# Optimization experiments

Measured on AMD Instinct MI355X. Metric: run time of the kernel, lower is better.

The kernel has to match this reference:

```python
import jax, jax.numpy as jnp
import numpy as np
import math

IN_FEATURES = 3072
PADDED = 4096  # next power of two
ACT_BITS = 8
LN_EPS = 1e-6


def hadamard_transform(x):
    """Normalized fast Walsh-Hadamard transform along last dim (power of 2)."""
    n = x.shape[-1]
    m = n.bit_length() - 1  # log2(n)
    shape = x.shape
    y = x.reshape(shape[:-1] + (2,) * m)
    for ax in range(len(shape) - 1, len(shape) - 1 + m):
        a = jnp.take(y, 0, axis=ax)
        b = jnp.take(y, 1, axis=ax)
        y = jnp.stack([a + b, a - b], axis=ax)
    return y.reshape(shape) / jnp.sqrt(jnp.asarray(n, x.dtype))


def activation_quant(x, bits=ACT_BITS):
    """Per-token absmax int-b quant with STE (BitNet style)."""
    qb = 2 ** (bits - 1) - 1  # 127
    scale = qb / jnp.clip(jnp.max(jnp.abs(x), axis=-1, keepdims=True), 1e-5)
    q = jnp.clip(jnp.round(x * scale), -qb - 1, qb) / scale
    return x + jax.lax.stop_gradient(q - x)


def weight_quant(w):
    """Ternary absmean weight quant with STE (as in training path)."""
    scale = jnp.clip(jnp.mean(jnp.abs(w)), 1e-5)
    q = jnp.clip(jnp.round(w / scale), -1.0, 1.0) * scale
    return w + jax.lax.stop_gradient(q - w)


def layer_norm(x, gamma, beta, eps=LN_EPS):
    mu = jnp.mean(x, axis=-1, keepdims=True)
    var = jnp.mean(jnp.square(x - mu), axis=-1, keepdims=True)
    return (x - mu) * jax.lax.rsqrt(var + eps) * gamma + beta


def setup_inputs() -> dict:
    key = jax.random.key(0)
    k1, k2 = jax.random.split(key)
    x = jax.random.normal(k1, (4, 2048, IN_FEATURES), dtype=jnp.float32)
    ln_gamma = jnp.ones((IN_FEATURES,), dtype=jnp.float32)
    ln_beta = jnp.zeros((IN_FEATURES,), dtype=jnp.float32)
    weight = jax.random.normal(k2, (4096, PADDED), dtype=jnp.float32) * 0.02
    return {"x": x, "ln_gamma": ln_gamma, "ln_beta": ln_beta, "weight": weight}


def reference(x, ln_gamma, ln_beta, weight):
    x_norm = layer_norm(x, ln_gamma, ln_beta)
    pad = PADDED - IN_FEATURES
    x_pad = jnp.pad(x_norm, ((0, 0), (0, 0), (0, pad)))
    x_had = hadamard_transform(x_pad)
    x_q = activation_quant(x_had)
    w_q = weight_quant(weight)
    # F.linear: x @ W^T
    out = jnp.einsum('bsd,od->bso', x_q, w_q)
    return out
```

## Files before the change

kernel.cpp:

```cpp
#include <hip/hip_runtime.h>
#include <stdint.h>

#define TOKENS 8192
#define IN_F   3072
#define PAD_F  4096
#define N_OUT  4096
#define K_DIM  4096

using i32x4 = __attribute__((ext_vector_type(4))) int;

#define Q_OFF    0
#define WQ_OFF   33554432
#define AINV_OFF 50331648
#define PART_OFF 50364416
#define WSC_OFF  50380800

__device__ __forceinline__ void gload_lds16(const void* g, void* l) {
    __builtin_amdgcn_global_load_lds(
        (__attribute__((address_space(1))) void*)(void*)g,
        (__attribute__((address_space(3))) void*)l,
        16, 0, 0);
}

__global__ __launch_bounds__(256) void k_wabs(const float* __restrict__ w,
                                              float* __restrict__ partial) {
    int tid = threadIdx.x;
    const float4* w4 = (const float4*)(w + (size_t)blockIdx.x * 4096);
    float s = 0.f;
#pragma unroll
    for (int i = 0; i < 4; ++i) {
        float4 v = w4[tid + i * 256];
        s += fabsf(v.x) + fabsf(v.y) + fabsf(v.z) + fabsf(v.w);
    }
#pragma unroll
    for (int o = 32; o > 0; o >>= 1) s += __shfl_xor(s, o);
    __shared__ float rb[4];
    if ((tid & 63) == 0) rb[tid >> 6] = s;
    __syncthreads();
    if (tid == 0) partial[blockIdx.x] = rb[0] + rb[1] + rb[2] + rb[3];
}

__global__ __launch_bounds__(256) void k_wscale(const float* __restrict__ partial,
                                                float* __restrict__ wsp) {
    int tid = threadIdx.x;
    float s = 0.f;
#pragma unroll
    for (int i = 0; i < 16; ++i) s += partial[tid + i * 256];
#pragma unroll
    for (int o = 32; o > 0; o >>= 1) s += __shfl_xor(s, o);
    __shared__ float rb[4];
    if ((tid & 63) == 0) rb[tid >> 6] = s;
    __syncthreads();
    if (tid == 0)
        wsp[0] = fmaxf((rb[0] + rb[1] + rb[2] + rb[3]) * (1.0f / 16777216.0f), 1e-5f);
}

__global__ __launch_bounds__(256) void k_wquant(const float* __restrict__ w,
                                                const float* __restrict__ wsp,
                                                unsigned int* __restrict__ wq) {
    int idx = blockIdx.x * 256 + threadIdx.x;
    float ws = wsp[0];
    float4 v = ((const float4*)w)[idx];
    int a = (int)rintf(v.x / ws); a = max(-1, min(1, a));
    int b = (int)rintf(v.y / ws); b = max(-1, min(1, b));
    int c = (int)rintf(v.z / ws); c = max(-1, min(1, c));
    int d = (int)rintf(v.w / ws); d = max(-1, min(1, d));
    unsigned int p = (unsigned)(a & 255) | ((unsigned)(b & 255) << 8) |
                     ((unsigned)(c & 255) << 16) | ((unsigned)(d & 255) << 24);
    wq[idx] = p;
}

__global__ __launch_bounds__(256) void k_lnfwht(const float* __restrict__ x,
                                                const float* __restrict__ gamma,
                                                const float* __restrict__ beta,
                                                signed char* __restrict__ q,
                                                float* __restrict__ ainv) {
    __shared__ float s[PAD_F];
    __shared__ float rb[8];
    int tid = threadIdx.x;
    int lane = tid & 63;
    int t = blockIdx.x;
    const float* xr = x + (size_t)t * IN_F;

    float v[16];
    float sum = 0.f;
#pragma unroll
    for (int i = 0; i < 12; ++i) { v[i] = xr[tid + i * 256]; sum += v[i]; }
    v[12] = v[13] = v[14] = v[15] = 0.f;
#pragma unroll
    for (int o = 32; o > 0; o >>= 1) sum += __shfl_xor(sum, o);
    if ((tid & 63) == 0) rb[tid >> 6] = sum;
    __syncthreads();
    float mu = (rb[0] + rb[1] + rb[2] + rb[3]) * (1.0f / 3072.0f);

    float s2 = 0.f;
#pragma unroll
    for (int i = 0; i < 12; ++i) { float d = v[i] - mu; s2 += d * d; }
#pragma unroll
    for (int o = 32; o > 0; o >>= 1) s2 += __shfl_xor(s2, o);
    if ((tid & 63) == 0) rb[4 + (tid >> 6)] = s2;
    __syncthreads();
    float var = (rb[4] + rb[5] + rb[6] + rb[7]) * (1.0f / 3072.0f);
    float rstd = 1.0f / sqrtf(var + 1e-6f);

#pragma unroll
    for (int i = 0; i < 12; ++i)
        v[i] = (v[i] - mu) * rstd * gamma[tid + i * 256] + beta[tid + i * 256];

#pragma unroll
    for (int b = 1; b < 16; b <<= 1) {
#pragma unroll
        for (int i = 0; i < 16; ++i) {
            if (!(i & b)) {
                float a0 = v[i], b0 = v[i | b];
                v[i] = a0 + b0;
                v[i | b] = a0 - b0;
            }
        }
    }
#pragma unroll
    for (int m = 1; m <= 32; m <<= 1) {
#pragma unroll
        for (int i = 0; i < 16; ++i) {
            float p = __shfl_xor(v[i], m);
            v[i] = (lane & m) ? (p - v[i]) : (v[i] + p);
        }
    }
#pragma unroll
    for (int m = 64; m <= 128; m <<= 1) {
        __syncthreads();
#pragma unroll
        for (int i = 0; i < 16; ++i) s[tid + i * 256] = v[i];
        __syncthreads();
#pragma unroll
        for (int i = 0; i < 16; ++i) {
            float p = s[(tid ^ m) + i * 256];
            v[i] = (tid & m) ? (p - v[i]) : (v[i] + p);
        }
    }

    float mx = 0.f;
#pragma unroll
    for (int i = 0; i < 16; ++i) mx = fmaxf(mx, fabsf(v[i]));
#pragma unroll
    for (int o = 32; o > 0; o >>= 1) mx = fmaxf(mx, __shfl_xor(mx, o));
    __syncthreads();
    if ((tid & 63) == 0) rb[tid >> 6] = mx;
    __syncthreads();
    float amraw = fmaxf(fmaxf(rb[0], rb[1]), fmaxf(rb[2], rb[3]));
    float amax = fmaxf(amraw * (1.0f / 64.0f), 1e-5f);
    float scale = 127.0f / amax;
    if (tid == 0) ainv[t] = amax * (1.0f / 127.0f);

    signed char* qr = q + (size_t)t * PAD_F;
#pragma unroll
    for (int i = 0; i < 16; ++i) {
        int qi = (int)rintf(v[i] * (1.0f / 64.0f) * scale);
        qi = max(-128, min(127, qi));
        qr[tid + i * 256] = (signed char)qi;
    }
}

#define BK 64
#define NT (K_DIM / BK)

#define VMW(n) asm volatile("s_waitcnt vmcnt(" #n ")" ::: "memory")

__global__ __launch_bounds__(512, 2) void k_gemm(const signed char* __restrict__ Aq,
                                                 const signed char* __restrict__ Wq,
                                                 const float* __restrict__ ainv,
                                                 const float* __restrict__ wsp,
                                                 float* __restrict__ out) {
    __shared__ signed char sA[4][128 * 128];
    __shared__ signed char sB[4][128 * 128];

    int tid = threadIdx.x;
    int lane = tid & 63, wid = tid >> 6;

    int bid = blockIdx.x;
    int xcd = bid & 7, li = bid >> 3;
    int bmb = xcd * 4 + (li & 3);
    int bnb = li >> 2;
    size_t bm0 = (size_t)bmb * 256, bn0 = (size_t)bnb * 256;

    int wm = wid >> 2, wn = wid & 3;

    int rr = lane >> 3, pp = lane & 7;
    int Lg = pp ^ rr;
    int spar = Lg >> 2, sh = Lg & 3;
    const signed char* gA = Aq + (bm0 + (size_t)(wid * 32 + 2 * rr + spar)) * K_DIM + sh * 16;
    const signed char* gB = Wq + (bn0 + (size_t)(wid * 32 + 2 * rr + spar)) * K_DIM + sh * 16;

    int fr = lane & 15, hh = lane >> 4;
    int pos = (((fr & 1) << 2) | hh) ^ (fr >> 1);
    int abase = (wm * 64 + (fr >> 1)) * 8 + pos;
    int bbase = (wn * 32 + (fr >> 1)) * 8 + pos;

    i32x4 acc[8][4];
#pragma unroll
    for (int m = 0; m < 8; ++m)
#pragma unroll
        for (int n = 0; n < 4; ++n) acc[m][n] = (i32x4){0, 0, 0, 0};

    i32x4 afA[8], bfA[4], afB[8], bfB[4];

    auto STAGE = [&](int b, int t) {
        size_t k0 = (size_t)t * BK;
        gload_lds16(gA + k0, &sA[b][(wid * 16) * 128]);
        gload_lds16(gA + k0 + (size_t)16 * K_DIM, &sA[b][(wid * 16 + 8) * 128]);
        gload_lds16(gB + k0, &sB[b][(wid * 16) * 128]);
        gload_lds16(gB + k0 + (size_t)16 * K_DIM, &sB[b][(wid * 16 + 8) * 128]);
    };

#define LOADF(B, AF, BF) do {                                           \
    const i32x4* va = (const i32x4*)&sA[B][0];                          \
    const i32x4* vb = (const i32x4*)&sB[B][0];                          \
    _Pragma("unroll")                                                   \
    for (int mf = 0; mf < 8; ++mf) AF[mf] = va[abase + mf * 64];        \
    _Pragma("unroll")                                                   \
    for (int nf = 0; nf < 4; ++nf) BF[nf] = vb[bbase + nf * 64];        \
} while (0)

#define COMPUTE(AF, BF) do {                                            \
    __builtin_amdgcn_s_setprio(1);                                      \
    _Pragma("unroll")                                                   \
    for (int mf = 0; mf < 8; ++mf)                                      \
        _Pragma("unroll")                                               \
        for (int nf = 0; nf < 4; ++nf)                                  \
            acc[mf][nf] = __builtin_amdgcn_mfma_i32_16x16x64_i8(        \
                AF[mf], BF[nf], acc[mf][nf], 0, 0, 0);                  \
    __builtin_amdgcn_s_setprio(0);                                      \
} while (0)

#define BODY(T, AFC, BFC, AFN, BFN) do {                                \
    STAGE((T + 3) & 3, T + 3);                                          \
    VMW(8);                                                             \
    __builtin_amdgcn_sched_barrier(0);                                  \
    __builtin_amdgcn_s_barrier();                                       \
    __builtin_amdgcn_sched_barrier(0);                                  \
    LOADF((T + 1) & 3, AFN, BFN);                                       \
    COMPUTE(AFC, BFC);                                                  \
    asm volatile("s_waitcnt lgkmcnt(0)" ::: "memory");                  \
    __builtin_amdgcn_sched_barrier(0);                                  \
} while (0)

    STAGE(0, 0);
    STAGE(1, 1);
    STAGE(2, 2);
    VMW(8);
    __builtin_amdgcn_sched_barrier(0);
    __builtin_amdgcn_s_barrier();
    __builtin_amdgcn_sched_barrier(0);
    LOADF(0, afA, bfA);
    asm volatile("s_waitcnt lgkmcnt(0)" ::: "memory");
    __builtin_amdgcn_sched_barrier(0);

#pragma unroll 1
    for (int t = 0; t < NT - 4; t += 2) {
        BODY(t, afA, bfA, afB, bfB);
        BODY(t + 1, afB, bfB, afA, bfA);
    }
    BODY(NT - 4, afA, bfA, afB, bfB);
    VMW(4);
    __builtin_amdgcn_sched_barrier(0);
    __builtin_amdgcn_s_barrier();
    __builtin_amdgcn_sched_barrier(0);
    LOADF(2, afA, bfA);
    COMPUTE(afB, bfB);
    asm volatile("s_waitcnt lgkmcnt(0)" ::: "memory");
    __builtin_amdgcn_sched_barrier(0);
    VMW(0);
    __builtin_amdgcn_sched_barrier(0);
    __builtin_amdgcn_s_barrier();
    __builtin_amdgcn_sched_barrier(0);
    LOADF(3, afB, bfB);
    COMPUTE(afA, bfA);
    asm volatile("s_waitcnt lgkmcnt(0)" ::: "memory");
    __builtin_amdgcn_sched_barrier(0);
    COMPUTE(afB, bfB);

    float wsc = wsp[0];
#pragma unroll
    for (int mf = 0; mf < 8; ++mf) {
        size_t row0 = bm0 + wm * 128 + mf * 16 + hh * 4;
#pragma unroll
        for (int r = 0; r < 4; ++r) {
            size_t row = row0 + r;
            float sa = wsc * ainv[row];
#pragma unroll
            for (int nf = 0; nf < 4; ++nf) {
                size_t col = bn0 + wn * 64 + nf * 16 + fr;
                out[row * N_OUT + col] = (float)acc[mf][nf][r] * sa;
            }
        }
    }
#undef LOADF
#undef COMPUTE
#undef BODY
}

extern "C" void kernel_launch(void* const* d_in, const int* in_sizes, int n_in,
                              void* d_out, int out_size, void* d_ws, size_t ws_size,
                              hipStream_t stream) {
    const float* x     = (const float*)d_in[0];
    const float* gamma = (const float*)d_in[1];
    const float* beta  = (const float*)d_in[2];
    const float* w     = (const float*)d_in[3];
    float* out = (float*)d_out;
    char* ws = (char*)d_ws;

    signed char* q   = (signed char*)(ws + Q_OFF);
    signed char* wq  = (signed char*)(ws + WQ_OFF);
    float* ainv      = (float*)(ws + AINV_OFF);
    float* partial   = (float*)(ws + PART_OFF);
    float* wsp       = (float*)(ws + WSC_OFF);

    k_wabs<<<dim3(4096), dim3(256), 0, stream>>>(w, partial);
    k_wscale<<<dim3(1), dim3(256), 0, stream>>>(partial, wsp);
    k_wquant<<<dim3(16384), dim3(256), 0, stream>>>(w, wsp, (unsigned int*)wq);
    k_lnfwht<<<dim3(TOKENS), dim3(256), 0, stream>>>(x, gamma, beta, q, ainv);
    k_gemm<<<dim3(512), dim3(512), 0, stream>>>(q, wq, ainv, wsp, out);
}
```

Measured before the change: 213.4 us.

## Use 4 waves with 128x128 warp tiles and interleave LDS loads with MFMAs

Cuts the GEMM block from 8 waves to 4, so each wave computes a 128x128 sub-tile (8x8 MFMA fragments) with larger accumulator and fragment arrays, and each wave issues twice as many global-to-LDS loads. The fragment loads for the next K-step are split into four chunks, each placed between groups of 16 MFMAs, and the pipeline tail is rewritten as conditional body steps. The goal is higher fragment reuse per wave and better overlap of LDS reads with matrix math. The cost is roughly doubled VGPR/AGPR pressure with launch bounds of one block, fewer waves per CU to hide latency, and a risk of spills.

```diff
diff --git a/kernel.cpp b/kernel.cpp
--- a/kernel.cpp
+++ b/kernel.cpp
@@ -165,8 +165,9 @@
 #define NT (K_DIM / BK)
 
 #define VMW(n) asm volatile("s_waitcnt vmcnt(" #n ")" ::: "memory")
-
-__global__ __launch_bounds__(512, 2) void k_gemm(const signed char* __restrict__ Aq,
+#define SB0()  __builtin_amdgcn_sched_barrier(0)
+
+__global__ __launch_bounds__(256, 1) void k_gemm(const signed char* __restrict__ Aq,
                                                  const signed char* __restrict__ Wq,
                                                  const float* __restrict__ ainv,
                                                  const float* __restrict__ wsp,
@@ -183,101 +184,99 @@
     int bnb = li >> 2;
     size_t bm0 = (size_t)bmb * 256, bn0 = (size_t)bnb * 256;
 
-    int wm = wid >> 2, wn = wid & 3;
+    int wm = wid >> 1, wn = wid & 1;
 
     int rr = lane >> 3, pp = lane & 7;
     int Lg = pp ^ rr;
     int spar = Lg >> 2, sh = Lg & 3;
-    const signed char* gA = Aq + (bm0 + (size_t)(wid * 32 + 2 * rr + spar)) * K_DIM + sh * 16;
-    const signed char* gB = Wq + (bn0 + (size_t)(wid * 32 + 2 * rr + spar)) * K_DIM + sh * 16;
+    const signed char* gA = Aq + (bm0 + (size_t)(wid * 64 + 2 * rr + spar)) * K_DIM + sh * 16;
+    const signed char* gB = Wq + (bn0 + (size_t)(wid * 64 + 2 * rr + spar)) * K_DIM + sh * 16;
 
     int fr = lane & 15, hh = lane >> 4;
     int pos = (((fr & 1) << 2) | hh) ^ (fr >> 1);
     int abase = (wm * 64 + (fr >> 1)) * 8 + pos;
-    int bbase = (wn * 32 + (fr >> 1)) * 8 + pos;
-
-    i32x4 acc[8][4];
+    int bbase = (wn * 64 + (fr >> 1)) * 8 + pos;
+
+    i32x4 acc[8][8];
 #pragma unroll
     for (int m = 0; m < 8; ++m)
 #pragma unroll
-        for (int n = 0; n < 4; ++n) acc[m][n] = (i32x4){0, 0, 0, 0};
-
-    i32x4 afA[8], bfA[4], afB[8], bfB[4];
+        for (int n = 0; n < 8; ++n) acc[m][n] = (i32x4){0, 0, 0, 0};
+
+    i32x4 afA[8], bfA[8], afB[8], bfB[8];
 
     auto STAGE = [&](int b, int t) {
         size_t k0 = (size_t)t * BK;
-        gload_lds16(gA + k0, &sA[b][(wid * 16) * 128]);
-        gload_lds16(gA + k0 + (size_t)16 * K_DIM, &sA[b][(wid * 16 + 8) * 128]);
-        gload_lds16(gB + k0, &sB[b][(wid * 16) * 128]);
-        gload_lds16(gB + k0 + (size_t)16 * K_DIM, &sB[b][(wid * 16 + 8) * 128]);
+#pragma unroll
+        for (int i = 0; i < 4; ++i) {
+            gload_lds16(gA + k0 + (size_t)i * 16 * K_DIM, &sA[b][(wid * 32 + i * 8) * 128]);
+            gload_lds16(gB + k0 + (size_t)i * 16 * K_DIM, &sB[b][(wid * 32 + i * 8) * 128]);
+        }
     };
 
-#define LOADF(B, AF, BF) do {                                           \
-    const i32x4* va = (const i32x4*)&sA[B][0];                          \
-    const i32x4* vb = (const i32x4*)&sB[B][0];                          \
+#define LOAD4(VP, BASE, AF, LO) do {                                    \
+    AF[LO]     = VP[BASE + (LO) * 64];                                  \
+    AF[LO + 1] = VP[BASE + (LO + 1) * 64];                              \
+    AF[LO + 2] = VP[BASE + (LO + 2) * 64];                              \
+    AF[LO + 3] = VP[BASE + (LO + 3) * 64];                              \
+} while (0)
+
+#define MFMA16(AF, BF, M0) do {                                         \
     _Pragma("unroll")                                                   \
-    for (int mf = 0; mf < 8; ++mf) AF[mf] = va[abase + mf * 64];        \
-    _Pragma("unroll")                                                   \
-    for (int nf = 0; nf < 4; ++nf) BF[nf] = vb[bbase + nf * 64];        \
+    for (int nf = 0; nf < 8; ++nf) {                                    \
+        acc[M0][nf] = __builtin_amdgcn_mfma_i32_16x16x64_i8(            \
+            AF[M0], BF[nf], acc[M0][nf], 0, 0, 0);                      \
+        acc[M0 + 1][nf] = __builtin_amdgcn_mfma_i32_16x16x64_i8(        \
+            AF[M0 + 1], BF[nf], acc[M0 + 1][nf], 0, 0, 0);              \
+    }                                                                   \
 } while (0)
 
-#define COMPUTE(AF, BF) do {                                            \
-    __builtin_amdgcn_s_setprio(1);                                      \
-    _Pragma("unroll")                                                   \
-    for (int mf = 0; mf < 8; ++mf)                                      \
-        _Pragma("unroll")                                               \
-        for (int nf = 0; nf < 4; ++nf)                                  \
-            acc[mf][nf] = __builtin_amdgcn_mfma_i32_16x16x64_i8(        \
-                AF[mf], BF[nf], acc[mf][nf], 0, 0, 0);                  \
-    __builtin_amdgcn_s_setprio(0);                                      \
-} while (0)
-
-#define BODY(T, AFC, BFC, AFN, BFN) do {                                \
-    STAGE((T + 3) & 3, T + 3);                                          \
-    VMW(8);                                                             \
-    __builtin_amdgcn_sched_barrier(0);                                  \
+#define BODYC(T, NW, DS, AFC, BFC, AFN, BFN) do {                       \
+    if (DS) STAGE((T + 3) & 3, T + 3);                                  \
+    VMW(NW);                                                            \
+    SB0();                                                              \
     __builtin_amdgcn_s_barrier();                                       \
-    __builtin_amdgcn_sched_barrier(0);                                  \
-    LOADF((T + 1) & 3, AFN, BFN);                                       \
-    COMPUTE(AFC, BFC);                                                  \
+    SB0();                                                              \
+    const i32x4* va = (const i32x4*)&sA[(T + 1) & 3][0];                \
+    const i32x4* vb = (const i32x4*)&sB[(T + 1) & 3][0];                \
+    LOAD4(va, abase, AFN, 0); SB0(); MFMA16(AFC, BFC, 0); SB0();        \
+    LOAD4(va, abase, AFN, 4); SB0(); MFMA16(AFC, BFC, 2); SB0();        \
+    LOAD4(vb, bbase, BFN, 0); SB0(); MFMA16(AFC, BFC, 4); SB0();        \
+    LOAD4(vb, bbase, BFN, 4); SB0(); MFMA16(AFC, BFC, 6); SB0();        \
     asm volatile("s_waitcnt lgkmcnt(0)" ::: "memory");                  \
-    __builtin_amdgcn_sched_barrier(0);                                  \
+    SB0();                                                              \
 } while (0)
 
     STAGE(0, 0);
     STAGE(1, 1);
     STAGE(2, 2);
-    VMW(8);
-    __builtin_amdgcn_sched_barrier(0);
+    VMW(16);
+    SB0();
     __builtin_amdgcn_s_barrier();
-    __builtin_amdgcn_sched_barrier(0);
-    LOADF(0, afA, bfA);
+    SB0();
+    {
+        const i32x4* va = (const i32x4*)&sA[0][0];
+        const i32x4* vb = (const i32x4*)&sB[0][0];
+        LOAD4(va, abase, afA, 0);
+        LOAD4(va, abase, afA, 4);
+        LOAD4(vb, bbase, bfA, 0);
+        LOAD4(vb, bbase, bfA, 4);
+    }
     asm volatile("s_waitcnt lgkmcnt(0)" ::: "memory");
-    __builtin_amdgcn_sched_barrier(0);
+    SB0();
 
 #pragma unroll 1
     for (int t = 0; t < NT - 4; t += 2) {
-        BODY(t, afA, bfA, afB, bfB);
-        BODY(t + 1, afB, bfB, afA, bfA);
-    }
-    BODY(NT - 4, afA, bfA, afB, bfB);
-    VMW(4);
-    __builtin_amdgcn_sched_barrier(0);
-    __builtin_amdgcn_s_barrier();
-    __builtin_amdgcn_sched_barrier(0);
-    LOADF(2, afA, bfA);
-    COMPUTE(afB, bfB);
-    asm volatile("s_waitcnt lgkmcnt(0)" ::: "memory");
-    __builtin_amdgcn_sched_barrier(0);
-    VMW(0);
-    __builtin_amdgcn_sched_barrier(0);
-    __builtin_amdgcn_s_barrier();
-    __builtin_amdgcn_sched_barrier(0);
-    LOADF(3, afB, bfB);
-    COMPUTE(afA, bfA);
-    asm volatile("s_waitcnt lgkmcnt(0)" ::: "memory");
-    __builtin_amdgcn_sched_barrier(0);
-    COMPUTE(afB, bfB);
+        BODYC(t, 16, true, afA, bfA, afB, bfB);
+        BODYC(t + 1, 16, true, afB, bfB, afA, bfA);
+    }
+    BODYC(NT - 4, 16, true, afA, bfA, afB, bfB);
+    BODYC(NT - 3, 8, false, afB, bfB, afA, bfA);
+    BODYC(NT - 2, 0, false, afA, bfA, afB, bfB);
+    MFMA16(afB, bfB, 0);
+    MFMA16(afB, bfB, 2);
+    MFMA16(afB, bfB, 4);
+    MFMA16(afB, bfB, 6);
 
     float wsc = wsp[0];
 #pragma unroll
@@ -288,15 +287,15 @@
             size_t row = row0 + r;
             float sa = wsc * ainv[row];
 #pragma unroll
-            for (int nf = 0; nf < 4; ++nf) {
-                size_t col = bn0 + wn * 64 + nf * 16 + fr;
+            for (int nf = 0; nf < 8; ++nf) {
+                size_t col = bn0 + wn * 128 + nf * 16 + fr;
                 out[row * N_OUT + col] = (float)acc[mf][nf][r] * sa;
             }
         }
     }
-#undef LOADF
-#undef COMPUTE
-#undef BODY
+#undef LOAD4
+#undef MFMA16
+#undef BODYC
 }
 
 extern "C" void kernel_launch(void* const* d_in, const int* in_sizes, int n_in,
@@ -319,5 +318,5 @@
     k_wscale<<<dim3(1), dim3(256), 0, stream>>>(partial, wsp);
     k_wquant<<<dim3(16384), dim3(256), 0, stream>>>(w, wsp, (unsigned int*)wq);
     k_lnfwht<<<dim3(TOKENS), dim3(256), 0, stream>>>(x, gamma, beta, q, ainv);
-    k_gemm<<<dim3(512), dim3(512), 0, stream>>>(q, wq, ainv, wsp, out);
-}
+    k_gemm<<<dim3(512), dim3(256), 0, stream>>>(q, wq, ainv, wsp, out);
+}
```

New measurement: 229.9 us. 7.7% more time.

## Shrink GEMM tile to 256x128, triple-buffer LDS, drop register double-buffering

Applied to the files above, without the earlier changes.

The int8 GEMM block tile drops from 256x256 to 256x128, with 2x4 waves each owning a 64x64 subtile, and the grid doubles to 1024 blocks. LDS staging goes from four buffers to three and the B tile is halved, and the register-level double buffering of fragments is replaced by a simple load-then-compute per K step. The aim is higher occupancy (launch bounds 512,4), less register pressure and LDS use, and more blocks to fill the CUs. The cost is lower arithmetic intensity per block, more global traffic for A, and less overlap of LDS reads with MFMA work.

```diff
diff --git a/kernel.cpp b/kernel.cpp
--- a/kernel.cpp
+++ b/kernel.cpp
@@ -165,14 +165,15 @@
 #define NT (K_DIM / BK)
 
 #define VMW(n) asm volatile("s_waitcnt vmcnt(" #n ")" ::: "memory")
-
-__global__ __launch_bounds__(512, 2) void k_gemm(const signed char* __restrict__ Aq,
+#define SB0()  __builtin_amdgcn_sched_barrier(0)
+
+__global__ __launch_bounds__(512, 4) void k_gemm(const signed char* __restrict__ Aq,
                                                  const signed char* __restrict__ Wq,
                                                  const float* __restrict__ ainv,
                                                  const float* __restrict__ wsp,
                                                  float* __restrict__ out) {
-    __shared__ signed char sA[4][128 * 128];
-    __shared__ signed char sB[4][128 * 128];
+    __shared__ signed char sA[3][128 * 128];
+    __shared__ signed char sB[3][64 * 128];
 
     int tid = threadIdx.x;
     int lane = tid & 63, wid = tid >> 6;
@@ -181,108 +182,79 @@
     int xcd = bid & 7, li = bid >> 3;
     int bmb = xcd * 4 + (li & 3);
     int bnb = li >> 2;
-    size_t bm0 = (size_t)bmb * 256, bn0 = (size_t)bnb * 256;
-
-    int wm = wid >> 2, wn = wid & 3;
+    size_t bm0 = (size_t)bmb * 256, bn0 = (size_t)bnb * 128;
+
+    int wm = wid >> 1, wn = wid & 1;
 
     int rr = lane >> 3, pp = lane & 7;
     int Lg = pp ^ rr;
     int spar = Lg >> 2, sh = Lg & 3;
     const signed char* gA = Aq + (bm0 + (size_t)(wid * 32 + 2 * rr + spar)) * K_DIM + sh * 16;
-    const signed char* gB = Wq + (bn0 + (size_t)(wid * 32 + 2 * rr + spar)) * K_DIM + sh * 16;
+    const signed char* gB = Wq + (bn0 + (size_t)(wid * 16 + 2 * rr + spar)) * K_DIM + sh * 16;
 
     int fr = lane & 15, hh = lane >> 4;
     int pos = (((fr & 1) << 2) | hh) ^ (fr >> 1);
-    int abase = (wm * 64 + (fr >> 1)) * 8 + pos;
+    int abase = (wm * 32 + (fr >> 1)) * 8 + pos;
     int bbase = (wn * 32 + (fr >> 1)) * 8 + pos;
 
-    i32x4 acc[8][4];
-#pragma unroll
-    for (int m = 0; m < 8; ++m)
+    i32x4 acc[4][4];
+#pragma unroll
+    for (int m = 0; m < 4; ++m)
 #pragma unroll
         for (int n = 0; n < 4; ++n) acc[m][n] = (i32x4){0, 0, 0, 0};
-
-    i32x4 afA[8], bfA[4], afB[8], bfB[4];
 
     auto STAGE = [&](int b, int t) {
         size_t k0 = (size_t)t * BK;
         gload_lds16(gA + k0, &sA[b][(wid * 16) * 128]);
         gload_lds16(gA + k0 + (size_t)16 * K_DIM, &sA[b][(wid * 16 + 8) * 128]);
-        gload_lds16(gB + k0, &sB[b][(wid * 16) * 128]);
-        gload_lds16(gB + k0 + (size_t)16 * K_DIM, &sB[b][(wid * 16 + 8) * 128]);
+        gload_lds16(gB + k0, &sB[b][(wid * 8) * 128]);
     };
 
-#define LOADF(B, AF, BF) do {                                           \
+#define TILE_COMPUTE(B) do {                                            \
     const i32x4* va = (const i32x4*)&sA[B][0];                          \
     const i32x4* vb = (const i32x4*)&sB[B][0];                          \
+    i32x4 af[4], bf[4];                                                 \
     _Pragma("unroll")                                                   \
-    for (int mf = 0; mf < 8; ++mf) AF[mf] = va[abase + mf * 64];        \
+    for (int mf = 0; mf < 4; ++mf) af[mf] = va[abase + mf * 64];        \
     _Pragma("unroll")                                                   \
-    for (int nf = 0; nf < 4; ++nf) BF[nf] = vb[bbase + nf * 64];        \
-} while (0)
-
-#define COMPUTE(AF, BF) do {                                            \
+    for (int nf = 0; nf < 4; ++nf) bf[nf] = vb[bbase + nf * 64];        \
     __builtin_amdgcn_s_setprio(1);                                      \
     _Pragma("unroll")                                                   \
-    for (int mf = 0; mf < 8; ++mf)                                      \
+    for (int mf = 0; mf < 4; ++mf)                                      \
         _Pragma("unroll")                                               \
         for (int nf = 0; nf < 4; ++nf)                                  \
             acc[mf][nf] = __builtin_amdgcn_mfma_i32_16x16x64_i8(        \
-                AF[mf], BF[nf], acc[mf][nf], 0, 0, 0);                  \
+                af[mf], bf[nf], acc[mf][nf], 0, 0, 0);                  \
     __builtin_amdgcn_s_setprio(0);                                      \
 } while (0)
 
-#define BODY(T, AFC, BFC, AFN, BFN) do {                                \
-    STAGE((T + 3) & 3, T + 3);                                          \
-    VMW(8);                                                             \
-    __builtin_amdgcn_sched_barrier(0);                                  \
-    __builtin_amdgcn_s_barrier();                                       \
-    __builtin_amdgcn_sched_barrier(0);                                  \
-    LOADF((T + 1) & 3, AFN, BFN);                                       \
-    COMPUTE(AFC, BFC);                                                  \
-    asm volatile("s_waitcnt lgkmcnt(0)" ::: "memory");                  \
-    __builtin_amdgcn_sched_barrier(0);                                  \
-} while (0)
-
     STAGE(0, 0);
     STAGE(1, 1);
-    STAGE(2, 2);
-    VMW(8);
-    __builtin_amdgcn_sched_barrier(0);
+    VMW(3);
+    SB0();
+
+#pragma unroll 1
+    for (int t = 0; t < NT - 2; ++t) {
+        __builtin_amdgcn_s_barrier();
+        SB0();
+        STAGE((t + 2) % 3, t + 2);
+        VMW(3);
+        SB0();
+        TILE_COMPUTE(t % 3);
+    }
     __builtin_amdgcn_s_barrier();
-    __builtin_amdgcn_sched_barrier(0);
-    LOADF(0, afA, bfA);
-    asm volatile("s_waitcnt lgkmcnt(0)" ::: "memory");
-    __builtin_amdgcn_sched_barrier(0);
-
-#pragma unroll 1
-    for (int t = 0; t < NT - 4; t += 2) {
-        BODY(t, afA, bfA, afB, bfB);
-        BODY(t + 1, afB, bfB, afA, bfA);
-    }
-    BODY(NT - 4, afA, bfA, afB, bfB);
-    VMW(4);
-    __builtin_amdgcn_sched_barrier(0);
+    SB0();
+    VMW(0);
+    SB0();
+    TILE_COMPUTE((NT - 2) % 3);
     __builtin_amdgcn_s_barrier();
-    __builtin_amdgcn_sched_barrier(0);
-    LOADF(2, afA, bfA);
-    COMPUTE(afB, bfB);
-    asm volatile("s_waitcnt lgkmcnt(0)" ::: "memory");
-    __builtin_amdgcn_sched_barrier(0);
-    VMW(0);
-    __builtin_amdgcn_sched_barrier(0);
-    __builtin_amdgcn_s_barrier();
-    __builtin_amdgcn_sched_barrier(0);
-    LOADF(3, afB, bfB);
-    COMPUTE(afA, bfA);
-    asm volatile("s_waitcnt lgkmcnt(0)" ::: "memory");
-    __builtin_amdgcn_sched_barrier(0);
-    COMPUTE(afB, bfB);
+    SB0();
+    TILE_COMPUTE((NT - 1) % 3);
 
     float wsc = wsp[0];
 #pragma unroll
-    for (int mf = 0; mf < 8; ++mf) {
-        size_t row0 = bm0 + wm * 128 + mf * 16 + hh * 4;
+    for (int mf = 0; mf < 4; ++mf) {
+        size_t row0 = bm0 + wm * 64 + mf * 16 + hh * 4;
 #pragma unroll
         for (int r = 0; r < 4; ++r) {
             size_t row = row0 + r;
@@ -294,9 +266,7 @@
             }
         }
     }
-#undef LOADF
-#undef COMPUTE
-#undef BODY
+#undef TILE_COMPUTE
 }
 
 extern "C" void kernel_launch(void* const* d_in, const int* in_sizes, int n_in,
@@ -319,5 +289,5 @@
     k_wscale<<<dim3(1), dim3(256), 0, stream>>>(partial, wsp);
     k_wquant<<<dim3(16384), dim3(256), 0, stream>>>(w, wsp, (unsigned int*)wq);
     k_lnfwht<<<dim3(TOKENS), dim3(256), 0, stream>>>(x, gamma, beta, q, ainv);
-    k_gemm<<<dim3(512), dim3(512), 0, stream>>>(q, wq, ainv, wsp, out);
-}
+    k_gemm<<<dim3(1024), dim3(512), 0, stream>>>(q, wq, ainv, wsp, out);
+}
```

After: 224.1 us. +5.0%, slower.

## Load B fragments directly from global into registers, bypassing LDS

Applied to the files above, without the earlier changes.

Removes the LDS staging buffer for the weight operand and has each wave load its B MFMA fragments directly from global memory one tile ahead. The A operand pipeline is shortened from three to two tiles in flight, with wait counts and the loop tail adjusted accordingly. This halves shared memory use, which may allow more blocks per CU and cuts LDS read traffic. In exchange, B is fetched redundantly by waves sharing columns, and global latency is less hidden.

```diff
diff --git a/kernel.cpp b/kernel.cpp
--- a/kernel.cpp
+++ b/kernel.cpp
@@ -165,6 +165,7 @@
 #define NT (K_DIM / BK)
 
 #define VMW(n) asm volatile("s_waitcnt vmcnt(" #n ")" ::: "memory")
+#define SB0()  __builtin_amdgcn_sched_barrier(0)
 
 __global__ __launch_bounds__(512, 2) void k_gemm(const signed char* __restrict__ Aq,
                                                  const signed char* __restrict__ Wq,
@@ -172,7 +173,6 @@
                                                  const float* __restrict__ wsp,
                                                  float* __restrict__ out) {
     __shared__ signed char sA[4][128 * 128];
-    __shared__ signed char sB[4][128 * 128];
 
     int tid = threadIdx.x;
     int lane = tid & 63, wid = tid >> 6;
@@ -189,12 +189,15 @@
     int Lg = pp ^ rr;
     int spar = Lg >> 2, sh = Lg & 3;
     const signed char* gA = Aq + (bm0 + (size_t)(wid * 32 + 2 * rr + spar)) * K_DIM + sh * 16;
-    const signed char* gB = Wq + (bn0 + (size_t)(wid * 32 + 2 * rr + spar)) * K_DIM + sh * 16;
 
     int fr = lane & 15, hh = lane >> 4;
     int pos = (((fr & 1) << 2) | hh) ^ (fr >> 1);
     int abase = (wm * 64 + (fr >> 1)) * 8 + pos;
-    int bbase = (wn * 32 + (fr >> 1)) * 8 + pos;
+
+    const signed char* bp0 = Wq + (bn0 + (size_t)(wn * 64 +  0 + fr)) * K_DIM + hh * 16;
+    const signed char* bp1 = Wq + (bn0 + (size_t)(wn * 64 + 16 + fr)) * K_DIM + hh * 16;
+    const signed char* bp2 = Wq + (bn0 + (size_t)(wn * 64 + 32 + fr)) * K_DIM + hh * 16;
+    const signed char* bp3 = Wq + (bn0 + (size_t)(wn * 64 + 48 + fr)) * K_DIM + hh * 16;
 
     i32x4 acc[8][4];
 #pragma unroll
@@ -202,23 +205,26 @@
 #pragma unroll
         for (int n = 0; n < 4; ++n) acc[m][n] = (i32x4){0, 0, 0, 0};
 
-    i32x4 afA[8], bfA[4], afB[8], bfB[4];
+    i32x4 afA[8], afB[8], bfA[4], bfB[4];
 
     auto STAGE = [&](int b, int t) {
         size_t k0 = (size_t)t * BK;
         gload_lds16(gA + k0, &sA[b][(wid * 16) * 128]);
         gload_lds16(gA + k0 + (size_t)16 * K_DIM, &sA[b][(wid * 16 + 8) * 128]);
-        gload_lds16(gB + k0, &sB[b][(wid * 16) * 128]);
-        gload_lds16(gB + k0 + (size_t)16 * K_DIM, &sB[b][(wid * 16 + 8) * 128]);
     };
 
-#define LOADF(B, AF, BF) do {                                           \
+#define LOADB(T, BF) do {                                               \
+    size_t k0 = (size_t)(T) * BK;                                       \
+    BF[0] = *(const i32x4*)(bp0 + k0);                                  \
+    BF[1] = *(const i32x4*)(bp1 + k0);                                  \
+    BF[2] = *(const i32x4*)(bp2 + k0);                                  \
+    BF[3] = *(const i32x4*)(bp3 + k0);                                  \
+} while (0)
+
+#define LOADFA(B, AF) do {                                              \
     const i32x4* va = (const i32x4*)&sA[B][0];                          \
-    const i32x4* vb = (const i32x4*)&sB[B][0];                          \
     _Pragma("unroll")                                                   \
     for (int mf = 0; mf < 8; ++mf) AF[mf] = va[abase + mf * 64];        \
-    _Pragma("unroll")                                                   \
-    for (int nf = 0; nf < 4; ++nf) BF[nf] = vb[bbase + nf * 64];        \
 } while (0)
 
 #define COMPUTE(AF, BF) do {                                            \
@@ -233,50 +239,45 @@
 } while (0)
 
 #define BODY(T, AFC, BFC, AFN, BFN) do {                                \
-    STAGE((T + 3) & 3, T + 3);                                          \
-    VMW(8);                                                             \
-    __builtin_amdgcn_sched_barrier(0);                                  \
+    STAGE((T + 2) & 3, T + 2);                                          \
+    LOADB(T + 1, BFN);                                                  \
+    VMW(6);                                                             \
+    SB0();                                                              \
     __builtin_amdgcn_s_barrier();                                       \
-    __builtin_amdgcn_sched_barrier(0);                                  \
-    LOADF((T + 1) & 3, AFN, BFN);                                       \
+    SB0();                                                              \
+    LOADFA((T + 1) & 3, AFN);                                           \
     COMPUTE(AFC, BFC);                                                  \
     asm volatile("s_waitcnt lgkmcnt(0)" ::: "memory");                  \
-    __builtin_amdgcn_sched_barrier(0);                                  \
+    SB0();                                                              \
 } while (0)
 
+    LOADB(0, bfA);
     STAGE(0, 0);
     STAGE(1, 1);
-    STAGE(2, 2);
-    VMW(8);
-    __builtin_amdgcn_sched_barrier(0);
+    VMW(2);
+    SB0();
     __builtin_amdgcn_s_barrier();
-    __builtin_amdgcn_sched_barrier(0);
-    LOADF(0, afA, bfA);
+    SB0();
+    LOADFA(0, afA);
     asm volatile("s_waitcnt lgkmcnt(0)" ::: "memory");
-    __builtin_amdgcn_sched_barrier(0);
+    SB0();
 
 #pragma unroll 1
-    for (int t = 0; t < NT - 4; t += 2) {
+    for (int t = 0; t < NT - 2; t += 2) {
         BODY(t, afA, bfA, afB, bfB);
         BODY(t + 1, afB, bfB, afA, bfA);
     }
-    BODY(NT - 4, afA, bfA, afB, bfB);
+    LOADB(63, bfB);
     VMW(4);
-    __builtin_amdgcn_sched_barrier(0);
+    SB0();
     __builtin_amdgcn_s_barrier();
-    __builtin_amdgcn_sched_barrier(0);
-    LOADF(2, afA, bfA);
-    COMPUTE(afB, bfB);
-    asm volatile("s_waitcnt lgkmcnt(0)" ::: "memory");
-    __builtin_amdgcn_sched_barrier(0);
-    VMW(0);
-    __builtin_amdgcn_sched_barrier(0);
-    __builtin_amdgcn_s_barrier();
-    __builtin_amdgcn_sched_barrier(0);
-    LOADF(3, afB, bfB);
+    SB0();
+    LOADFA(3, afB);
     COMPUTE(afA, bfA);
     asm volatile("s_waitcnt lgkmcnt(0)" ::: "memory");
-    __builtin_amdgcn_sched_barrier(0);
+    SB0();
+    VMW(0);
+    SB0();
     COMPUTE(afB, bfB);
 
     float wsc = wsp[0];
@@ -294,7 +295,8 @@
             }
         }
     }
-#undef LOADF
+#undef LOADB
+#undef LOADFA
 #undef COMPUTE
 #undef BODY
 }
```

Result: slower. 240.3 us (+12.6%).
